# Kernel optimization log

Hardware: AMD Instinct MI355X
Metric: run time of the kernel (lower is better)

## Reference

```python
import jax, jax.numpy as jnp
import numpy as np

N_SLICES = 2  # init kwarg n_slices


def affine_grid_3d(theta, D, H, W):
    """torch.nn.functional.affine_grid for 5D output, align_corners=False.
    theta: [B,3,4]; returns grid [B,D,H,W,3] with last dim (x,y,z) ~ (W,H,D)."""
    xs = (jnp.arange(W, dtype=theta.dtype) + 0.5) * (2.0 / W) - 1.0
    ys = (jnp.arange(H, dtype=theta.dtype) + 0.5) * (2.0 / H) - 1.0
    zs = (jnp.arange(D, dtype=theta.dtype) + 0.5) * (2.0 / D) - 1.0
    zz, yy, xx = jnp.meshgrid(zs, ys, xs, indexing='ij')
    base = jnp.stack([xx, yy, zz, jnp.ones_like(xx)], axis=-1)  # [D,H,W,4]
    return jnp.einsum('bij,dhwj->bdhwi', theta, base)  # [B,D,H,W,3]


def grid_sample_3d_zeros(vol, grid):
    """torch.nn.functional.grid_sample, mode='bilinear' (trilinear for 5D),
    padding_mode='zeros', align_corners=False.
    vol: [B,C,D,H,W]; grid: [B,D,H,W,3] normalized xyz coords."""
    B, C, D, H, W = vol.shape
    ix = ((grid[..., 0] + 1.0) * W - 1.0) * 0.5
    iy = ((grid[..., 1] + 1.0) * H - 1.0) * 0.5
    iz = ((grid[..., 2] + 1.0) * D - 1.0) * 0.5
    ix0 = jnp.floor(ix); iy0 = jnp.floor(iy); iz0 = jnp.floor(iz)
    fx = ix - ix0; fy = iy - iy0; fz = iz - iz0

    def gather(v, z, y, x):  # v: [C,D,H,W], idx: [D,H,W] -> [C,D,H,W]
        return v[:, z, y, x]

    out = jnp.zeros((B, C, D, H, W), vol.dtype)
    for dz in (0, 1):
        for dy in (0, 1):
            for dx in (0, 1):
                xi = ix0 + dx; yi = iy0 + dy; zi = iz0 + dz
                w = (jnp.where(dx, fx, 1.0 - fx)
                     * jnp.where(dy, fy, 1.0 - fy)
                     * jnp.where(dz, fz, 1.0 - fz))
                valid = ((xi >= 0) & (xi < W) & (yi >= 0) & (yi < H)
                         & (zi >= 0) & (zi < D))
                xc = jnp.clip(xi, 0, W - 1).astype(jnp.int32)
                yc = jnp.clip(yi, 0, H - 1).astype(jnp.int32)
                zc = jnp.clip(zi, 0, D - 1).astype(jnp.int32)
                vals = jax.vmap(gather)(vol, zc, yc, xc)  # [B,C,D,H,W]
                out = out + vals * (w * valid)[:, None]
    return out


def skip_connector(x, b_grid_affines):
    B, C, SPAT, _ = x.shape
    # zero volume with the 2D slice stack placed at the central W-plane
    vol = jnp.zeros((B, C, SPAT, SPAT, SPAT), x.dtype).at[..., SPAT // 2].set(x)
    chunks = jnp.split(vol, N_SLICES, axis=1)
    outs = []
    for i in range(N_SLICES):
        aff = b_grid_affines[i].astype(jnp.float32)  # [B,4,4]
        # get_zooms: column norms of rotation block
        zooms = jnp.sqrt((aff[:, :3, :3] ** 2).sum(axis=1))  # [B,3]
        # rescale_rot_components_with_diag(aff, 1/zooms) == aff @ diag(1/zx,1/zy,1/zz,1)
        scale = jnp.concatenate([1.0 / zooms, jnp.ones((aff.shape[0], 1), aff.dtype)], axis=1)
        aff = aff * scale[:, None, :]
        theta = jnp.linalg.inv(aff)[:, :3, :]  # [B,3,4]
        grid = affine_grid_3d(theta, SPAT, SPAT, SPAT)
        outs.append(grid_sample_3d_zeros(chunks[i], grid))
    return jnp.concatenate(outs, axis=1)  # [B,C,SPAT,SPAT,SPAT]


def setup_inputs() -> dict:
    key = jax.random.key(0)
    k1, k2 = jax.random.split(key)
    B, C, SPAT = 2, 32, 96
    x = jax.random.normal(k1, (B, C, SPAT, SPAT), dtype=jnp.float32)
    # near-identity invertible homogeneous affines for the two views (SA, HLA)
    noise = 0.1 * jax.random.normal(k2, (2, B, 4, 4), dtype=jnp.float32)
    aff = jnp.eye(4, dtype=jnp.float32)[None, None] + noise
    aff = aff.at[..., 3, :].set(jnp.array([0.0, 0.0, 0.0, 1.0], dtype=jnp.float32))
    return {"x": x, "b_grid_affines": aff}


def reference(x, b_grid_affines):
    return skip_connector(x, b_grid_affines)
```

## Files before the change

### kernel.cpp

```cpp
#include <hip/hip_runtime.h>
#include <math.h>

#define SPAT  96
#define IMG   (SPAT*SPAT)
#define PLANE (SPAT*SPAT*SPAT)
#define CC_CH (PLANE/4)
#define D_CH  (IMG/4)
#define NCHUNK (64u*CC_CH)
#define KSLOT 3
#define STAGE_F4 (4*16*IMG*KSLOT)
#define STAGE_BYTES ((size_t)STAGE_F4*16)
#define NROWS (4*IMG)
#define WS_NEED (STAGE_BYTES + (size_t)NROWS*4)

#define HROWS 48
#define HCHUNK (HROWS*24)

__device__ inline void invert4(const float m[16], float inv[16]) {
    inv[0]  =  m[5]*m[10]*m[15] - m[5]*m[11]*m[14] - m[9]*m[6]*m[15] + m[9]*m[7]*m[14] + m[13]*m[6]*m[11] - m[13]*m[7]*m[10];
    inv[4]  = -m[4]*m[10]*m[15] + m[4]*m[11]*m[14] + m[8]*m[6]*m[15] - m[8]*m[7]*m[14] - m[12]*m[6]*m[11] + m[12]*m[7]*m[10];
    inv[8]  =  m[4]*m[9]*m[15]  - m[4]*m[11]*m[13] - m[8]*m[5]*m[15] + m[8]*m[7]*m[13] + m[12]*m[5]*m[11] - m[12]*m[7]*m[9];
    inv[12] = -m[4]*m[9]*m[14]  + m[4]*m[10]*m[13] + m[8]*m[5]*m[14] - m[8]*m[6]*m[13] - m[12]*m[5]*m[10] + m[12]*m[6]*m[9];
    inv[1]  = -m[1]*m[10]*m[15] + m[1]*m[11]*m[14] + m[9]*m[2]*m[15] - m[9]*m[3]*m[14] - m[13]*m[2]*m[11] + m[13]*m[3]*m[10];
    inv[5]  =  m[0]*m[10]*m[15] - m[0]*m[11]*m[14] - m[8]*m[2]*m[15] + m[8]*m[3]*m[14] + m[12]*m[2]*m[11] - m[12]*m[3]*m[10];
    inv[9]  = -m[0]*m[9]*m[15]  + m[0]*m[11]*m[13] + m[8]*m[1]*m[15] - m[8]*m[3]*m[13] - m[12]*m[1]*m[11] + m[12]*m[3]*m[9];
    inv[13] =  m[0]*m[9]*m[14]  - m[0]*m[10]*m[13] - m[8]*m[1]*m[14] + m[8]*m[2]*m[13] + m[12]*m[1]*m[10] - m[12]*m[2]*m[9];
    inv[2]  =  m[1]*m[6]*m[15]  - m[1]*m[7]*m[14]  - m[5]*m[2]*m[15] + m[5]*m[3]*m[14] + m[13]*m[2]*m[7]  - m[13]*m[3]*m[6];
    inv[6]  = -m[0]*m[6]*m[15]  + m[0]*m[7]*m[14]  + m[4]*m[2]*m[15] - m[4]*m[3]*m[14] - m[12]*m[2]*m[7]  + m[12]*m[3]*m[6];
    inv[10] =  m[0]*m[5]*m[15]  - m[0]*m[7]*m[13]  - m[4]*m[1]*m[15] + m[4]*m[3]*m[13] + m[12]*m[1]*m[7]  - m[12]*m[3]*m[5];
    inv[14] = -m[0]*m[5]*m[14]  + m[0]*m[6]*m[13]  + m[4]*m[1]*m[14] - m[4]*m[2]*m[13] - m[12]*m[1]*m[6]  + m[12]*m[2]*m[5];
    inv[3]  = -m[1]*m[6]*m[11]  + m[1]*m[7]*m[10]  + m[5]*m[2]*m[11] - m[5]*m[3]*m[10] - m[9]*m[2]*m[7]   + m[9]*m[3]*m[6];
    inv[7]  =  m[0]*m[6]*m[11]  - m[0]*m[7]*m[10]  - m[4]*m[2]*m[11] + m[4]*m[3]*m[10] + m[8]*m[2]*m[7]   - m[8]*m[3]*m[6];
    inv[11] = -m[0]*m[5]*m[11]  + m[0]*m[7]*m[9]   + m[4]*m[1]*m[11] - m[4]*m[3]*m[9]  - m[8]*m[1]*m[7]   + m[8]*m[3]*m[5];
    inv[15] =  m[0]*m[5]*m[10]  - m[0]*m[6]*m[9]   - m[4]*m[1]*m[10] + m[4]*m[2]*m[9]  + m[8]*m[1]*m[6]   - m[8]*m[2]*m[5];
    float det  = m[0]*inv[0] + m[1]*inv[4] + m[2]*inv[8] + m[3]*inv[12];
    float rdet = 1.0f / det;
    for (int i = 0; i < 16; ++i) inv[i] *= rdet;
}

__device__ inline void fold_affine(const float* __restrict__ aff_in, int sb,
                                   float M[12]) {
    float A[16];
    #pragma unroll
    for (int i = 0; i < 16; ++i) A[i] = aff_in[sb * 16 + i];
    #pragma unroll
    for (int j = 0; j < 3; ++j) {
        float z = sqrtf(A[0*4+j]*A[0*4+j] + A[1*4+j]*A[1*4+j] + A[2*4+j]*A[2*4+j]);
        float rz = 1.0f / z;
        #pragma unroll
        for (int i = 0; i < 4; ++i) A[i*4+j] *= rz;
    }
    float inv[16];
    invert4(A, inv);
    #pragma unroll
    for (int r = 0; r < 3; ++r) {
        float T0 = inv[r*4+0], T1 = inv[r*4+1], T2 = inv[r*4+2], T3 = inv[r*4+3];
        M[r*4+0] = T0;
        M[r*4+1] = T1;
        M[r*4+2] = T2;
        M[r*4+3] = -47.5f * (T0 + T1 + T2) + 48.0f * T3 + 47.5f;
    }
}

__global__ __launch_bounds__(128) void prep_kernel(
        const float* __restrict__ xin,
        const float* __restrict__ aff_in,
        float4* __restrict__ stage,
        unsigned* __restrict__ rowinfo,
        float* __restrict__ outp) {
    const int tid = (int)threadIdx.x;
    if (tid >= SPAT) return;
    const int d  = blockIdx.x;
    const int sb = blockIdx.y;
    const int h  = tid;

    float M[12];
    fold_affine(aff_in, sb, M);
    const float Mxw = M[0], Mxh = M[1], Mxd = M[2],  Mx0 = M[3];
    const float Myw = M[4], Myh = M[5], Myd = M[6],  My0 = M[7];
    const float Mzw = M[8], Mzh = M[9], Mzd = M[10], Mz0 = M[11];

    const float fh = (float)h, fd = (float)d;
    const float bx = Mxh * fh + Mxd * fd + Mx0;

    int wlo, whi;
    if (fabsf(Mxw) > 1e-6f) {
        float rMxw = 1.0f / Mxw;
        float w1 = (47.0f - bx) * rMxw;
        float w2 = (49.0f - bx) * rMxw;
        float wmin = fminf(w1, w2), wmax = fmaxf(w1, w2);
        wlo = max((int)ceilf(wmin), 0);
        whi = min((int)floorf(wmax), SPAT - 1);
    } else {
        bool in = fabsf(bx - 48.0f) < 1.0f;
        wlo = in ? 0 : 1;
        whi = in ? SPAT - 1 : 0;
    }

    const int rix = (sb * SPAT + d) * SPAT + h;
    if (wlo > whi) { rowinfo[rix] = 0xFFu; return; }
    const int qlo = wlo >> 2, qhi = whi >> 2;
    const bool ovf = (qhi - qlo + 1) > KSLOT;
    rowinfo[rix] = (unsigned)qlo | ((unsigned)qhi << 8) | (ovf ? 0x10000u : 0u);

    const int s = sb >> 1, b = sb & 1;
    const float* imgbase = xin + (size_t)(b * 32 + s * 16) * IMG;
    const float by = Myh * fh + Myd * fd + My0;
    const float bz = Mzh * fh + Mzd * fd + Mz0;

    for (int q = qlo; q <= qhi; ++q) {
        float wt[4][4];
        int   of[4][4];
        #pragma unroll
        for (int j = 0; j < 4; ++j) {
            float fw = (float)(4 * q + j);
            float ix = Mxw * fw + bx;
            float wx = 1.0f - fabsf(ix - 48.0f);
            if (wx > 0.0f) {
                float iy = Myw * fw + by;
                float iz = Mzw * fw + bz;
                float yf = floorf(iy), zf = floorf(iz);
                float fy = iy - yf,    fz = iz - zf;
                int y0 = (int)yf, z0 = (int)zf;
                bool vy0 = (y0 >= 0)  & (y0 <  SPAT);
                bool vy1 = (y0 >= -1) & (y0 <  SPAT - 1);
                bool vz0 = (z0 >= 0)  & (z0 <  SPAT);
                bool vz1 = (z0 >= -1) & (z0 <  SPAT - 1);
                int y0c = min(max(y0, 0),     SPAT - 1);
                int y1c = min(max(y0 + 1, 0), SPAT - 1);
                int z0c = min(max(z0, 0),     SPAT - 1);
                int z1c = min(max(z0 + 1, 0), SPAT - 1);
                float wy0 = 1.0f - fy, wy1 = fy;
                float wz0 = 1.0f - fz, wz1 = fz;
                wt[j][0] = wx * wz0 * wy0 * ((vz0 & vy0) ? 1.0f : 0.0f);
                wt[j][1] = wx * wz0 * wy1 * ((vz0 & vy1) ? 1.0f : 0.0f);
                wt[j][2] = wx * wz1 * wy0 * ((vz1 & vy0) ? 1.0f : 0.0f);
                wt[j][3] = wx * wz1 * wy1 * ((vz1 & vy1) ? 1.0f : 0.0f);
                of[j][0] = z0c * SPAT + y0c;  of[j][1] = z0c * SPAT + y1c;
                of[j][2] = z1c * SPAT + y0c;  of[j][3] = z1c * SPAT + y1c;
            } else {
                wt[j][0] = wt[j][1] = wt[j][2] = wt[j][3] = 0.0f;
                of[j][0] = of[j][1] = of[j][2] = of[j][3] = 0;
            }
        }
        if (!ovf) {
            const int k = q - qlo;
            #pragma unroll
            for (int ct = 0; ct < 16; ++ct) {
                const float* ic = imgbase + (size_t)ct * IMG;
                float4 v;
                v.x = wt[0][0]*ic[of[0][0]] + wt[0][1]*ic[of[0][1]] + wt[0][2]*ic[of[0][2]] + wt[0][3]*ic[of[0][3]];
                v.y = wt[1][0]*ic[of[1][0]] + wt[1][1]*ic[of[1][1]] + wt[1][2]*ic[of[1][2]] + wt[1][3]*ic[of[1][3]];
                v.z = wt[2][0]*ic[of[2][0]] + wt[2][1]*ic[of[2][1]] + wt[2][2]*ic[of[2][2]] + wt[2][3]*ic[of[2][3]];
                v.w = wt[3][0]*ic[of[3][0]] + wt[3][1]*ic[of[3][1]] + wt[3][2]*ic[of[3][2]] + wt[3][3]*ic[of[3][3]];
                stage[((size_t)(sb * 16 + ct) * IMG + (size_t)d * SPAT + h) * KSLOT + k] = v;
            }
        } else {
            #pragma unroll
            for (int ct = 0; ct < 16; ++ct) {
                const float* ic = imgbase + (size_t)ct * IMG;
                float4 v;
                v.x = wt[0][0]*ic[of[0][0]] + wt[0][1]*ic[of[0][1]] + wt[0][2]*ic[of[0][2]] + wt[0][3]*ic[of[0][3]];
                v.y = wt[1][0]*ic[of[1][0]] + wt[1][1]*ic[of[1][1]] + wt[1][2]*ic[of[1][2]] + wt[1][3]*ic[of[1][3]];
                v.z = wt[2][0]*ic[of[2][0]] + wt[2][1]*ic[of[2][1]] + wt[2][2]*ic[of[2][2]] + wt[2][3]*ic[of[2][3]];
                v.w = wt[3][0]*ic[of[3][0]] + wt[3][1]*ic[of[3][1]] + wt[3][2]*ic[of[3][2]] + wt[3][3]*ic[of[3][3]];
                *reinterpret_cast<float4*>(outp
                    + (size_t)(b * 32 + s * 16 + ct) * PLANE
                    + ((size_t)d * SPAT + h) * SPAT + 4 * q) = v;
            }
        }
    }
}

__global__ __launch_bounds__(256) void stream_kernel(
        const float4* __restrict__ stage,
        const unsigned* __restrict__ rowinfo,
        float4* __restrict__ out) {
    size_t i = (size_t)blockIdx.x * 256 + threadIdx.x;
    const size_t stride = (size_t)gridDim.x * 256;
    for (; i < (size_t)NCHUNK; i += stride) {
        unsigned ii = (unsigned)i;
        unsigned cc = ii / CC_CH;
        unsigned r1 = ii - cc * CC_CH;
        unsigned dd = r1 / D_CH;
        unsigned r2 = r1 - dd * D_CH;
        unsigned hh = r2 / 24u;
        unsigned q  = r2 - hh * 24u;
        unsigned sb = ((cc >> 4) & 1u) * 2u + (cc >> 5);
        unsigned info = rowinfo[(sb * SPAT + dd) * SPAT + hh];
        unsigned qlo = info & 0xFFu;
        unsigned qhi = (info >> 8) & 0xFFu;
        bool ins = (q >= qlo) && (q <= qhi);
        bool ovf = (info >> 16) != 0u;
        float4 v = make_float4(0.f, 0.f, 0.f, 0.f);
        if (ins && !ovf)
            v = stage[((size_t)(sb * 16u + (cc & 15u)) * IMG
                       + (size_t)dd * SPAT + hh) * KSLOT + (q - qlo)];
        if (!(ins && ovf))
            out[i] = v;
    }
}

__global__ __launch_bounds__(256, 4) void fused4_kernel(
        const float* __restrict__ xin,
        const float* __restrict__ aff_in,
        float4* __restrict__ out) {
    __shared__ float4 tile[HCHUNK];
    const int tid = (int)threadIdx.x;
    const int dh2 = blockIdx.x;
    const int d   = dh2 >> 1;
    const int hh  = dh2 & 1;
    const int cc  = blockIdx.y;
    const int b   = cc >> 5;
    const int s   = (cc >> 4) & 1;
    const int sb  = s * 2 + b;

    float M[12];
    fold_affine(aff_in, sb, M);
    const float Mxw = M[0], Mxh = M[1], Mxd = M[2],  Mx0 = M[3];
    const float Myw = M[4], Myh = M[5], Myd = M[6],  My0 = M[7];
    const float Mzw = M[8], Mzh = M[9], Mzd = M[10], Mz0 = M[11];

    const float* img = xin + (size_t)cc * IMG;

    float tv[16];
    float bx = 0.f, by = 0.f, bz = 0.f;
    int   rr = 0, myq = 0, fqlo = 0, fqhi = -1;
    bool  act = false;
    if (tid < 2 * HROWS) {
        rr = tid >> 1;
        const int k = tid & 1;
        const int h = hh * HROWS + rr;
        const float fh = (float)h, fd = (float)d;
        bx = Mxh * fh + Mxd * fd + Mx0;
        by = Myh * fh + Myd * fd + My0;
        bz = Mzh * fh + Mzd * fd + Mz0;

        int wlo, whi;
        if (fabsf(Mxw) > 1e-6f) {
            float rMxw = 1.0f / Mxw;
            float w1 = (47.0f - bx) * rMxw;
            float w2 = (49.0f - bx) * rMxw;
            float wmin = fminf(w1, w2), wmax = fmaxf(w1, w2);
            wlo = max((int)ceilf(wmin), 0);
            whi = min((int)floorf(wmax), SPAT - 1);
        } else {
            bool in = fabsf(bx - 48.0f) < 1.0f;
            wlo = in ? 0 : 1;
            whi = in ? SPAT - 1 : 0;
        }
        const int qlo = wlo >> 2, qhi = whi >> 2;
        myq = qlo + k;
        if (wlo <= whi && myq <= qhi) {
            act = true;
            #pragma unroll
            for (int j = 0; j < 4; ++j) {
                float fw = (float)(4 * myq + j);
                float ix = Mxw * fw + bx;
                float wx = 1.0f - fabsf(ix - 48.0f);
                if (wx > 0.0f) {
                    float iy = Myw * fw + by;
                    float iz = Mzw * fw + bz;
                    int y0 = (int)floorf(iy), z0 = (int)floorf(iz);
                    int y0c = min(max(y0, 0),     SPAT - 1);
                    int y1c = min(max(y0 + 1, 0), SPAT - 1);
                    int z0c = min(max(z0, 0),     SPAT - 1);
                    int z1c = min(max(z0 + 1, 0), SPAT - 1);
                    tv[4*j+0] = img[z0c * SPAT + y0c];
                    tv[4*j+1] = img[z0c * SPAT + y1c];
                    tv[4*j+2] = img[z1c * SPAT + y0c];
                    tv[4*j+3] = img[z1c * SPAT + y1c];
                } else {
                    tv[4*j+0] = 0.f; tv[4*j+1] = 0.f;
                    tv[4*j+2] = 0.f; tv[4*j+3] = 0.f;
                }
            }
        }
        if (k == 1 && wlo <= whi) { fqlo = qlo + 2; fqhi = qhi; }
    }

    const float4 z4 = make_float4(0.f, 0.f, 0.f, 0.f);
    #pragma unroll
    for (int i = tid; i < HCHUNK; i += 256) tile[i] = z4;

    __syncthreads();

    if (act) {
        float vv[4];
        #pragma unroll
        for (int j = 0; j < 4; ++j) {
            float fw = (float)(4 * myq + j);
            float ix = Mxw * fw + bx;
            float wx = 1.0f - fabsf(ix - 48.0f);
            float r = 0.0f;
            if (wx > 0.0f) {
                float iy = Myw * fw + by;
                float iz = Mzw * fw + bz;
                float yf = floorf(iy), zf = floorf(iz);
                float fy = iy - yf,    fz = iz - zf;
                int y0 = (int)yf, z0 = (int)zf;
                bool vy0 = (y0 >= 0)  & (y0 <  SPAT);
                bool vy1 = (y0 >= -1) & (y0 <  SPAT - 1);
                bool vz0 = (z0 >= 0)  & (z0 <  SPAT);
                bool vz1 = (z0 >= -1) & (z0 <  SPAT - 1);
                float wy0 = 1.0f - fy, wy1 = fy;
                float wz0 = 1.0f - fz, wz1 = fz;
                float w00 = wx * wz0 * wy0 * ((vz0 & vy0) ? 1.0f : 0.0f);
                float w01 = wx * wz0 * wy1 * ((vz0 & vy1) ? 1.0f : 0.0f);
                float w10 = wx * wz1 * wy0 * ((vz1 & vy0) ? 1.0f : 0.0f);
                float w11 = wx * wz1 * wy1 * ((vz1 & vy1) ? 1.0f : 0.0f);
                r = w00 * tv[4*j+0] + w01 * tv[4*j+1]
                  + w10 * tv[4*j+2] + w11 * tv[4*j+3];
            }
            vv[j] = r;
        }
        tile[rr * 24 + myq] = make_float4(vv[0], vv[1], vv[2], vv[3]);
    }
    for (int q = fqlo; q <= fqhi; ++q) {
        float vv[4];
        #pragma unroll
        for (int j = 0; j < 4; ++j) {
            float fw = (float)(4 * q + j);
            float ix = Mxw * fw + bx;
            float wx = 1.0f - fabsf(ix - 48.0f);
            float r = 0.0f;
            if (wx > 0.0f) {
                float iy = Myw * fw + by;
                float iz = Mzw * fw + bz;
                float yf = floorf(iy), zf = floorf(iz);
                float fy = iy - yf,    fz = iz - zf;
                int y0 = (int)yf, z0 = (int)zf;
                bool vy0 = (y0 >= 0)  & (y0 <  SPAT);
                bool vy1 = (y0 >= -1) & (y0 <  SPAT - 1);
                bool vz0 = (z0 >= 0)  & (z0 <  SPAT);
                bool vz1 = (z0 >= -1) & (z0 <  SPAT - 1);
                int y0c = min(max(y0, 0),     SPAT - 1);
                int y1c = min(max(y0 + 1, 0), SPAT - 1);
                int z0c = min(max(z0, 0),     SPAT - 1);
                int z1c = min(max(z0 + 1, 0), SPAT - 1);
                float wy0 = 1.0f - fy, wy1 = fy;
                float wz0 = 1.0f - fz, wz1 = fz;
                float w00 = wx * wz0 * wy0 * ((vz0 & vy0) ? 1.0f : 0.0f);
                float w01 = wx * wz0 * wy1 * ((vz0 & vy1) ? 1.0f : 0.0f);
                float w10 = wx * wz1 * wy0 * ((vz1 & vy0) ? 1.0f : 0.0f);
                float w11 = wx * wz1 * wy1 * ((vz1 & vy1) ? 1.0f : 0.0f);
                r = w00 * img[z0c * SPAT + y0c] + w01 * img[z0c * SPAT + y1c]
                  + w10 * img[z1c * SPAT + y0c] + w11 * img[z1c * SPAT + y1c];
            }
            vv[j] = r;
        }
        tile[rr * 24 + q] = make_float4(vv[0], vv[1], vv[2], vv[3]);
    }

    __syncthreads();

    float4* op = out + ((size_t)cc * (PLANE / 4) + (size_t)d * (IMG / 4)
                        + (size_t)hh * HCHUNK);
    #pragma unroll
    for (int i = tid; i < HCHUNK; i += 256) op[i] = tile[i];
}

extern "C" void kernel_launch(void* const* d_in, const int* in_sizes, int n_in,
                              void* d_out, int out_size, void* d_ws, size_t ws_size,
                              hipStream_t stream) {
    const float* x   = (const float*)d_in[0];
    const float* aff = (const float*)d_in[1];
    float* out = (float*)d_out;

    if (d_ws != nullptr && ws_size >= WS_NEED) {
        float4*   stage   = (float4*)d_ws;
        unsigned* rowinfo = (unsigned*)((char*)d_ws + STAGE_BYTES);
        dim3 pgrid(SPAT, 4);
        prep_kernel<<<pgrid, 128, 0, stream>>>(x, aff, stage, rowinfo, out);
        stream_kernel<<<4096, 256, 0, stream>>>(stage, rowinfo, (float4*)out);
    } else {
        dim3 grid(2 * SPAT, 64);
        fused4_kernel<<<grid, 256, 0, stream>>>(x, aff, (float4*)out);
    }
}
```

Before: 255.9 us.

## Parallelize prep over channels and stage rows through shared memory in stream pass

The prep kernel now assigns one thread per (slice-batch, channel, d, h) row instead of looping over 16 channels per thread, raising the thread count from 384 useful threads per block-row to a 2304-block grid. The stream kernel becomes one block per (d, channel) plane that loads that plane's staged values and row info into shared memory, then writes the full 96x24 float4 slab with a fixed 9-iteration loop. This replaces the per-element div/mod decode and scattered global stage reads. The prep stage had too little parallelism, which hid gather latency poorly. In exchange the sampling coordinates are recomputed for every channel.

```diff
diff --git a/kernel.cpp b/kernel.cpp
--- a/kernel.cpp
+++ b/kernel.cpp
@@ -4,12 +4,9 @@
 #define SPAT  96
 #define IMG   (SPAT*SPAT)
 #define PLANE (SPAT*SPAT*SPAT)
-#define CC_CH (PLANE/4)
-#define D_CH  (IMG/4)
-#define NCHUNK (64u*CC_CH)
 #define KSLOT 3
-#define STAGE_F4 (4*16*IMG*KSLOT)
-#define STAGE_BYTES ((size_t)STAGE_F4*16)
+#define STAGE_F4 ((size_t)4*16*IMG*KSLOT)
+#define STAGE_BYTES (STAGE_F4*16)
 #define NROWS (4*IMG)
 #define WS_NEED (STAGE_BYTES + (size_t)NROWS*4)
 
@@ -62,17 +59,20 @@
     }
 }
 
-__global__ __launch_bounds__(128) void prep_kernel(
+__global__ __launch_bounds__(256) void prep2_kernel(
         const float* __restrict__ xin,
         const float* __restrict__ aff_in,
         float4* __restrict__ stage,
         unsigned* __restrict__ rowinfo,
         float* __restrict__ outp) {
-    const int tid = (int)threadIdx.x;
-    if (tid >= SPAT) return;
-    const int d  = blockIdx.x;
-    const int sb = blockIdx.y;
-    const int h  = tid;
+    const int n  = (int)blockIdx.x * 256 + (int)threadIdx.x;
+    const int h  = n % SPAT;
+    const int t1 = n / SPAT;
+    const int d  = t1 % SPAT;
+    const int t2 = t1 / SPAT;
+    const int ct = t2 & 15;
+    const int sb = t2 >> 4;
+    const int s  = sb >> 1, b = sb & 1;
 
     float M[12];
     fold_affine(aff_in, sb, M);
@@ -96,27 +96,31 @@
         wlo = in ? 0 : 1;
         whi = in ? SPAT - 1 : 0;
     }
-
-    const int rix = (sb * SPAT + d) * SPAT + h;
-    if (wlo > whi) { rowinfo[rix] = 0xFFu; return; }
     const int qlo = wlo >> 2, qhi = whi >> 2;
-    const bool ovf = (qhi - qlo + 1) > KSLOT;
-    rowinfo[rix] = (unsigned)qlo | ((unsigned)qhi << 8) | (ovf ? 0x10000u : 0u);
-
-    const int s = sb >> 1, b = sb & 1;
-    const float* imgbase = xin + (size_t)(b * 32 + s * 16) * IMG;
-    const float by = Myh * fh + Myd * fd + My0;
-    const float bz = Mzh * fh + Mzd * fd + Mz0;
+    const bool empty = (wlo > whi);
+    const bool ovf = !empty && ((qhi - qlo + 1) > KSLOT);
+
+    if (ct == 0) {
+        const int rix = (sb * SPAT + d) * SPAT + h;
+        rowinfo[rix] = empty ? 0xFFu
+            : ((unsigned)qlo | ((unsigned)qhi << 8) | (ovf ? 0x10000u : 0u));
+    }
+    if (empty) return;
+
+    const int c_glob = b * 32 + s * 16 + ct;
+    const float* img = xin + (size_t)c_glob * IMG;
 
     for (int q = qlo; q <= qhi; ++q) {
-        float wt[4][4];
-        int   of[4][4];
+        float vv[4];
         #pragma unroll
         for (int j = 0; j < 4; ++j) {
             float fw = (float)(4 * q + j);
             float ix = Mxw * fw + bx;
             float wx = 1.0f - fabsf(ix - 48.0f);
+            float r = 0.0f;
             if (wx > 0.0f) {
+                float by = Myh * fh + Myd * fd + My0;
+                float bz = Mzh * fh + Mzd * fd + Mz0;
                 float iy = Myw * fw + by;
                 float iz = Mzw * fw + bz;
                 float yf = floorf(iy), zf = floorf(iz);
@@ -132,72 +136,62 @@
                 int z1c = min(max(z0 + 1, 0), SPAT - 1);
                 float wy0 = 1.0f - fy, wy1 = fy;
                 float wz0 = 1.0f - fz, wz1 = fz;
-                wt[j][0] = wx * wz0 * wy0 * ((vz0 & vy0) ? 1.0f : 0.0f);
-                wt[j][1] = wx * wz0 * wy1 * ((vz0 & vy1) ? 1.0f : 0.0f);
-                wt[j][2] = wx * wz1 * wy0 * ((vz1 & vy0) ? 1.0f : 0.0f);
-                wt[j][3] = wx * wz1 * wy1 * ((vz1 & vy1) ? 1.0f : 0.0f);
-                of[j][0] = z0c * SPAT + y0c;  of[j][1] = z0c * SPAT + y1c;
-                of[j][2] = z1c * SPAT + y0c;  of[j][3] = z1c * SPAT + y1c;
-            } else {
-                wt[j][0] = wt[j][1] = wt[j][2] = wt[j][3] = 0.0f;
-                of[j][0] = of[j][1] = of[j][2] = of[j][3] = 0;
+                float w00 = wx * wz0 * wy0 * ((vz0 & vy0) ? 1.0f : 0.0f);
+                float w01 = wx * wz0 * wy1 * ((vz0 & vy1) ? 1.0f : 0.0f);
+                float w10 = wx * wz1 * wy0 * ((vz1 & vy0) ? 1.0f : 0.0f);
+                float w11 = wx * wz1 * wy1 * ((vz1 & vy1) ? 1.0f : 0.0f);
+                r = w00 * img[z0c * SPAT + y0c] + w01 * img[z0c * SPAT + y1c]
+                  + w10 * img[z1c * SPAT + y0c] + w11 * img[z1c * SPAT + y1c];
             }
-        }
+            vv[j] = r;
+        }
+        float4 v = make_float4(vv[0], vv[1], vv[2], vv[3]);
         if (!ovf) {
-            const int k = q - qlo;
-            #pragma unroll
-            for (int ct = 0; ct < 16; ++ct) {
-                const float* ic = imgbase + (size_t)ct * IMG;
-                float4 v;
-                v.x = wt[0][0]*ic[of[0][0]] + wt[0][1]*ic[of[0][1]] + wt[0][2]*ic[of[0][2]] + wt[0][3]*ic[of[0][3]];
-                v.y = wt[1][0]*ic[of[1][0]] + wt[1][1]*ic[of[1][1]] + wt[1][2]*ic[of[1][2]] + wt[1][3]*ic[of[1][3]];
-                v.z = wt[2][0]*ic[of[2][0]] + wt[2][1]*ic[of[2][1]] + wt[2][2]*ic[of[2][2]] + wt[2][3]*ic[of[2][3]];
-                v.w = wt[3][0]*ic[of[3][0]] + wt[3][1]*ic[of[3][1]] + wt[3][2]*ic[of[3][2]] + wt[3][3]*ic[of[3][3]];
-                stage[((size_t)(sb * 16 + ct) * IMG + (size_t)d * SPAT + h) * KSLOT + k] = v;
-            }
+            stage[((size_t)t2 * IMG + (size_t)d * SPAT + h) * KSLOT
+                  + (q - qlo)] = v;
         } else {
-            #pragma unroll
-            for (int ct = 0; ct < 16; ++ct) {
-                const float* ic = imgbase + (size_t)ct * IMG;
-                float4 v;
-                v.x = wt[0][0]*ic[of[0][0]] + wt[0][1]*ic[of[0][1]] + wt[0][2]*ic[of[0][2]] + wt[0][3]*ic[of[0][3]];
-                v.y = wt[1][0]*ic[of[1][0]] + wt[1][1]*ic[of[1][1]] + wt[1][2]*ic[of[1][2]] + wt[1][3]*ic[of[1][3]];
-                v.z = wt[2][0]*ic[of[2][0]] + wt[2][1]*ic[of[2][1]] + wt[2][2]*ic[of[2][2]] + wt[2][3]*ic[of[2][3]];
-                v.w = wt[3][0]*ic[of[3][0]] + wt[3][1]*ic[of[3][1]] + wt[3][2]*ic[of[3][2]] + wt[3][3]*ic[of[3][3]];
-                *reinterpret_cast<float4*>(outp
-                    + (size_t)(b * 32 + s * 16 + ct) * PLANE
-                    + ((size_t)d * SPAT + h) * SPAT + 4 * q) = v;
-            }
-        }
-    }
-}
-
-__global__ __launch_bounds__(256) void stream_kernel(
+            *reinterpret_cast<float4*>(outp + (size_t)c_glob * PLANE
+                + ((size_t)d * SPAT + h) * SPAT + 4 * q) = v;
+        }
+    }
+}
+
+__global__ __launch_bounds__(256) void stream2_kernel(
         const float4* __restrict__ stage,
         const unsigned* __restrict__ rowinfo,
         float4* __restrict__ out) {
-    size_t i = (size_t)blockIdx.x * 256 + threadIdx.x;
-    const size_t stride = (size_t)gridDim.x * 256;
-    for (; i < (size_t)NCHUNK; i += stride) {
-        unsigned ii = (unsigned)i;
-        unsigned cc = ii / CC_CH;
-        unsigned r1 = ii - cc * CC_CH;
-        unsigned dd = r1 / D_CH;
-        unsigned r2 = r1 - dd * D_CH;
-        unsigned hh = r2 / 24u;
-        unsigned q  = r2 - hh * 24u;
-        unsigned sb = ((cc >> 4) & 1u) * 2u + (cc >> 5);
-        unsigned info = rowinfo[(sb * SPAT + dd) * SPAT + hh];
-        unsigned qlo = info & 0xFFu;
-        unsigned qhi = (info >> 8) & 0xFFu;
-        bool ins = (q >= qlo) && (q <= qhi);
-        bool ovf = (info >> 16) != 0u;
-        float4 v = make_float4(0.f, 0.f, 0.f, 0.f);
-        if (ins && !ovf)
-            v = stage[((size_t)(sb * 16u + (cc & 15u)) * IMG
-                       + (size_t)dd * SPAT + hh) * KSLOT + (q - qlo)];
+    __shared__ float4   sval[SPAT * KSLOT];
+    __shared__ unsigned rinf[SPAT];
+    const int tid = (int)threadIdx.x;
+    const int d   = blockIdx.x;
+    const int cc  = blockIdx.y;
+    const int b   = cc >> 5;
+    const int s   = (cc >> 4) & 1;
+    const int sb  = s * 2 + b;
+
+    const float4* sp = stage
+        + ((size_t)(sb * 16 + (cc & 15)) * IMG + (size_t)d * SPAT) * KSLOT;
+    for (int i = tid; i < SPAT * KSLOT; i += 256) sval[i] = sp[i];
+    if (tid < SPAT) rinf[tid] = rowinfo[(sb * SPAT + d) * SPAT + tid];
+    __syncthreads();
+
+    float4* op = out + (size_t)cc * (PLANE / 4) + (size_t)d * (IMG / 4);
+    #pragma unroll
+    for (int it = 0; it < 9; ++it) {
+        const int tl = tid + 256 * it;
+        const unsigned h = (unsigned)tl / 24u;
+        const unsigned q = (unsigned)tl - h * 24u;
+        const unsigned info = rinf[h];
+        const unsigned qlo = info & 0xFFu;
+        const unsigned qhi = (info >> 8) & 0xFFu;
+        const bool ins = (q >= qlo) & (q <= qhi);
+        const bool ovf = (info & 0x10000u) != 0u;
+        int slot = min(max((int)q - (int)qlo, 0), KSLOT - 1);
+        float4 sv = sval[h * KSLOT + slot];
+        float4 v = make_float4(ins ? sv.x : 0.f, ins ? sv.y : 0.f,
+                               ins ? sv.z : 0.f, ins ? sv.w : 0.f);
         if (!(ins && ovf))
-            out[i] = v;
+            op[tl] = v;
     }
 }
 
@@ -370,9 +364,9 @@
     if (d_ws != nullptr && ws_size >= WS_NEED) {
         float4*   stage   = (float4*)d_ws;
         unsigned* rowinfo = (unsigned*)((char*)d_ws + STAGE_BYTES);
-        dim3 pgrid(SPAT, 4);
-        prep_kernel<<<pgrid, 128, 0, stream>>>(x, aff, stage, rowinfo, out);
-        stream_kernel<<<4096, 256, 0, stream>>>(stage, rowinfo, (float4*)out);
+        prep2_kernel<<<2304, 256, 0, stream>>>(x, aff, stage, rowinfo, out);
+        dim3 sgrid(SPAT, 64);
+        stream2_kernel<<<sgrid, 256, 0, stream>>>(stage, rowinfo, (float4*)out);
     } else {
         dim3 grid(2 * SPAT, 64);
         fused4_kernel<<<grid, 256, 0, stream>>>(x, aff, (float4*)out);
```

Measured after the change: 241.6 us. 1.06x faster.
